# Optimization experiments

Hardware: AMD Instinct MI355X
Metric: run time of the kernel (lower is better)

## Reference

```python
import jax, jax.numpy as jnp
import numpy as np

B, T, C = 4, 2048, 2048
H, HKV, D = 16, 8, 128
SECTIONS = (24, 20, 20)  # sums to 64 = D/2 -> full-dim rotation branch
EPS = 1e-6


def setup_inputs() -> dict:
    key = jax.random.key(0)
    ks = jax.random.split(key, 8)
    x = jax.random.normal(ks[0], (B, T, C), dtype=jnp.float32)
    # realistic RoPE tables: [3, B, T, 64] (3 mRoPE axes: t/h/w)
    half = sum(SECTIONS)  # 64
    inv_freq = 1.0 / (10000.0 ** (jnp.arange(half, dtype=jnp.float32) / half))
    pos = jnp.arange(T, dtype=jnp.float32)
    freqs = pos[:, None] * inv_freq[None, :]                      # [T, 64]
    freqs3 = jnp.broadcast_to(freqs, (3, B, T, half))
    # small per-axis offsets so the three mRoPE axes differ
    axis_off = jnp.arange(3, dtype=jnp.float32)[:, None, None, None] * 0.5
    cos = jnp.cos(freqs3 + axis_off)
    sin = jnp.sin(freqs3 + axis_off)
    mask = jnp.ones((B, T), dtype=jnp.int32)
    s = 1.0 / np.sqrt(C)
    Wq = jax.random.normal(ks[1], (C, H * D), dtype=jnp.float32) * s
    Wk = jax.random.normal(ks[2], (C, HKV * D), dtype=jnp.float32) * s
    Wv = jax.random.normal(ks[3], (C, HKV * D), dtype=jnp.float32) * s
    Wo = jax.random.normal(ks[4], (H * D, C), dtype=jnp.float32) * (1.0 / np.sqrt(H * D))
    return dict(x=x, cos=cos, sin=sin, mask=mask,
                Wq=Wq, bq=jnp.zeros((H * D,), jnp.float32),
                Wk=Wk, bk=jnp.zeros((HKV * D,), jnp.float32),
                Wv=Wv, bv=jnp.zeros((HKV * D,), jnp.float32),
                gq=jnp.ones((D,), jnp.float32), gk=jnp.ones((D,), jnp.float32),
                Wo=Wo)


def _rms_norm(x, gamma, eps):
    var = jnp.mean(jnp.square(x.astype(jnp.float32)), axis=-1, keepdims=True)
    return (gamma * x * jax.lax.rsqrt(var + eps)).astype(x.dtype)


def _rotate_half(x):
    x1, x2 = jnp.split(x, 2, axis=-1)
    return jnp.concatenate((-x2, x1), axis=-1)


def _reorder(table):
    # interleave mRoPE sections: take section i from axis i, then duplicate
    chunks, off = [], 0
    for i, sec in enumerate(SECTIONS):
        chunks.append(table[i, ..., off:off + sec])
        off += sec
    r = jnp.concatenate(chunks, axis=-1)        # [B, T, 64]
    return jnp.concatenate([r, r], axis=-1)     # [B, T, 128]


def reference(x, cos, sin, mask, Wq, bq, Wk, bk, Wv, bv, gq, gk, Wo):
    b, t = x.shape[0], x.shape[1]
    q = (x @ Wq + bq).reshape(b, t, H, D)
    k = (x @ Wk + bk).reshape(b, t, HKV, D)
    v = (x @ Wv + bv).reshape(b, t, HKV, D)
    q = _rms_norm(q, gq, EPS)
    k = _rms_norm(k, gk, EPS)
    q = jnp.transpose(q, (0, 2, 1, 3))   # [B, H, T, D]
    k = jnp.transpose(k, (0, 2, 1, 3))   # [B, HKV, T, D]
    v = jnp.transpose(v, (0, 2, 1, 3))
    cos_e = _reorder(cos)[:, None].astype(q.dtype)  # [B, 1, T, D]
    sin_e = _reorder(sin)[:, None].astype(q.dtype)
    q = q * cos_e + _rotate_half(q) * sin_e
    k = k * cos_e + _rotate_half(k) * sin_e
    key_mask = mask.astype(jnp.float32)                         # [B, T]
    lengths = key_mask.sum(axis=-1).astype(jnp.int32)           # [B]
    k = k * key_mask[:, None, :, None].astype(k.dtype)
    v = v * key_mask[:, None, :, None].astype(v.dtype)
    history_mask = (jnp.arange(t)[None, :] < lengths[:, None]).astype(jnp.float32)
    repeats = H // HKV
    qg = q.reshape(b, HKV, repeats, t, D)
    scores = jnp.einsum('bhgqd,bhkd->bhgqk', qg.astype(jnp.float32),
                        k.astype(jnp.float32)) * D ** -0.5
    scores = scores.reshape(b, H, t, t)
    scores = scores + (1.0 - history_mask)[:, None, None, :] * -1e9
    causal = jnp.tril(jnp.ones((t, t), dtype=jnp.float32))
    scores = scores + (1.0 - causal)[None, None] * -1e9
    weights = jax.nn.softmax(scores, axis=-1)
    wg = weights.reshape(b, HKV, repeats, t, t)
    out = jnp.einsum('bhgqk,bhkd->bhgqd', wg, v.astype(jnp.float32))
    out = out.reshape(b, H, t, D).astype(x.dtype)
    out = jnp.transpose(out, (0, 2, 1, 3)).reshape(b, t, H * D)
    return out @ Wo
```

## Files before the change

### kernel.cpp

```cpp
#include <hip/hip_runtime.h>
#include <stdint.h>

#define B_    4
#define T_    2048
#define C_    2048
#define H_    16
#define HKV_  8
#define D_    128
#define HD_   2048
#define KVD_  1024
#define NQKV_ 4096
#define BT_   8192

typedef __bf16 bf16x8 __attribute__((ext_vector_type(8)));
typedef float  f32x4  __attribute__((ext_vector_type(4)));
typedef unsigned short u16;
typedef unsigned int   u32;

__device__ __forceinline__ u16 f2b(float f){
  union { float f; u32 u; } v; v.f = f;
  u32 r = v.u + 0x7FFFu + ((v.u >> 16) & 1u);
  return (u16)(r >> 16);
}
__device__ __forceinline__ float b2f(u16 h){
  union { u32 u; float f; } v; v.u = ((u32)h) << 16;
  return v.f;
}

#define GLOAD16(src, dst) __builtin_amdgcn_global_load_lds( \
    (const __attribute__((address_space(1))) u32*)(src), \
    (__attribute__((address_space(3))) u32*)(dst), 16, 0, 0)

#define MFMA16(a,b,c) __builtin_amdgcn_mfma_f32_16x16x32_bf16((a), (b), (c), 0, 0, 0)

__global__ __launch_bounds__(256) void k_convx(const float* __restrict__ x, u16* __restrict__ xb){
  size_t i = ((size_t)blockIdx.x * 256 + threadIdx.x) * 4;
  float4 v = *(const float4*)(x + i);
  u32 w0 = (u32)f2b(v.x) | ((u32)f2b(v.y) << 16);
  u32 w1 = (u32)f2b(v.z) | ((u32)f2b(v.w) << 16);
  uint2 pk; pk.x = w0; pk.y = w1;
  *(uint2*)(xb + i) = pk;
}

__global__ __launch_bounds__(256) void k_wtrans(const float* __restrict__ src, u16* __restrict__ dst,
                                                int K, int N){
  __shared__ __attribute__((aligned(16))) u16 tile[64][68];
  int n0 = blockIdx.x * 64, k0 = blockIdx.y * 64;
  int r = threadIdx.x >> 4, c4 = (threadIdx.x & 15) * 4;
  #pragma unroll
  for (int rr = 0; rr < 4; ++rr){
    int kl = r + rr * 16;
    float4 v = *(const float4*)(src + (size_t)(k0 + kl) * N + n0 + c4);
    tile[kl][c4+0] = f2b(v.x); tile[kl][c4+1] = f2b(v.y);
    tile[kl][c4+2] = f2b(v.z); tile[kl][c4+3] = f2b(v.w);
  }
  __syncthreads();
  #pragma unroll
  for (int rr = 0; rr < 4; ++rr){
    int nl = r + rr * 16;
    u32 w0 = (u32)tile[c4+0][nl] | ((u32)tile[c4+1][nl] << 16);
    u32 w1 = (u32)tile[c4+2][nl] | ((u32)tile[c4+3][nl] << 16);
    uint2 pk; pk.x = w0; pk.y = w1;
    *(uint2*)(dst + (size_t)(n0 + nl) * K + k0 + c4) = pk;
  }
}

__global__ void k_prep(const float* __restrict__ bq, const float* __restrict__ bk,
                       const float* __restrict__ bv, float* __restrict__ bias){
  int i = blockIdx.x * 256 + threadIdx.x;
  if (i < NQKV_)
    bias[i] = (i < HD_) ? bq[i] : (i < HD_ + KVD_ ? bk[i - HD_] : bv[i - HD_ - KVD_]);
}

__global__ void k_lens(const int* __restrict__ mask, int* __restrict__ lens){
  int b = blockIdx.x;
  int s = 0;
  for (int t = threadIdx.x; t < T_; t += 256) s += mask[b * T_ + t];
  #pragma unroll
  for (int d = 1; d < 64; d <<= 1) s += __shfl_xor(s, d);
  __shared__ int acc[4];
  if ((threadIdx.x & 63) == 0) acc[threadIdx.x >> 6] = s;
  __syncthreads();
  if (threadIdx.x == 0) lens[b] = acc[0] + acc[1] + acc[2] + acc[3];
}

template<bool OUTF32>
__global__ __launch_bounds__(256) void k_gemm(const u16* __restrict__ A, const u16* __restrict__ BT,
                                              const float* __restrict__ bias, void* __restrict__ Cout,
                                              int M, int N, int K, int nbx){
  __shared__ __attribute__((aligned(16))) u16 As[2][128 * 64];
  __shared__ __attribute__((aligned(16))) u16 Bs[2][128 * 64];
  int nwg = gridDim.x;
  int fid = blockIdx.x;
  int gs = (fid & 7) * (nwg >> 3) + (fid >> 3);
  int bx = gs % nbx, by = gs / nbx;
  int m0 = by * 128, n0 = bx * 128;
  int tid = threadIdx.x;
  int lane = tid & 63, w = tid >> 6;
  int wr = w >> 1, wc = w & 1;
  int g = lane >> 4, lo = lane & 15;
  int srow = lane >> 3;
  int sgr  = (lane & 7) ^ srow;
  int lsx  = (lo & 7) << 3;
  f32x4 acc[4][4] = {};

  auto STAGE = [&](int k0, int bufi){
    #pragma unroll
    for (int c = 0; c < 4; ++c){
      int ch = w * 4 + c;
      int row = ch * 8 + srow;
      GLOAD16(A + (size_t)(m0 + row) * K + k0 + sgr * 8, &As[bufi][ch * 512]);
    }
    #pragma unroll
    for (int c = 0; c < 4; ++c){
      int ch = w * 4 + c;
      int row = ch * 8 + srow;
      GLOAD16(BT + (size_t)(n0 + row) * K + k0 + sgr * 8, &Bs[bufi][ch * 512]);
    }
  };

  int nk = K >> 6;
  STAGE(0, 0);
  int cur = 0;
  for (int t = 0; t < nk; ++t){
    if (t + 1 < nk){
      STAGE((t + 1) * 64, cur ^ 1);
      asm volatile("s_waitcnt vmcnt(8)" ::: "memory");
    } else {
      asm volatile("s_waitcnt vmcnt(0)" ::: "memory");
    }
    __builtin_amdgcn_s_barrier();
    __builtin_amdgcn_sched_barrier(0);
    #pragma unroll
    for (int kk = 0; kk < 2; ++kk){
      bf16x8 af[4], bfv[4];
      #pragma unroll
      for (int i = 0; i < 4; ++i)
        af[i] = *(const bf16x8*)&As[cur][(wr*64 + i*16 + lo) * 64 + ((kk*32 + g*8) ^ lsx)];
      #pragma unroll
      for (int j = 0; j < 4; ++j)
        bfv[j] = *(const bf16x8*)&Bs[cur][(wc*64 + j*16 + lo) * 64 + ((kk*32 + g*8) ^ lsx)];
      __builtin_amdgcn_s_setprio(1);
      #pragma unroll
      for (int i = 0; i < 4; ++i)
        #pragma unroll
        for (int j = 0; j < 4; ++j)
          acc[i][j] = MFMA16(af[i], bfv[j], acc[i][j]);
      __builtin_amdgcn_s_setprio(0);
    }
    __builtin_amdgcn_s_barrier();
    cur ^= 1;
  }
  #pragma unroll
  for (int i = 0; i < 4; ++i){
    #pragma unroll
    for (int j = 0; j < 4; ++j){
      #pragma unroll
      for (int r = 0; r < 4; ++r){
        int row = m0 + wr*64 + i*16 + g*4 + r;
        int col = n0 + wc*64 + j*16 + lo;
        float v = acc[i][j][r] + (bias ? bias[col] : 0.0f);
        if (OUTF32) ((float*)Cout)[(size_t)row * N + col] = v;
        else        ((u16*)Cout)[(size_t)row * N + col] = f2b(v);
      }
    }
  }
}

__global__ __launch_bounds__(256) void k_rmsrope(const u16* __restrict__ qkv,
    const float* __restrict__ cosp, const float* __restrict__ sinp,
    const int* __restrict__ mask, const float* __restrict__ gq, const float* __restrict__ gk,
    u16* __restrict__ qrot, u16* __restrict__ krot){
  const float QS = 0.08838834764831845f * 1.4426950408889634f;
  int tok = blockIdx.x;
  int b = tok >> 11, t = tok & (T_ - 1);
  int lane = threadIdx.x & 63, w = threadIdx.x >> 6;
  int dl = (lane & 31) * 2;
  int a0 = dl < 24 ? 0 : (dl < 44 ? 1 : 2);
  int a1 = (dl + 1) < 24 ? 0 : ((dl + 1) < 44 ? 1 : 2);
  size_t cb = ((size_t)b * T_ + t) * 64;
  const size_t AX = (size_t)B_ * T_ * 64;
  float ce0 = cosp[(size_t)a0 * AX + cb + dl],     se0 = sinp[(size_t)a0 * AX + cb + dl];
  float ce1 = cosp[(size_t)a1 * AX + cb + dl + 1], se1 = sinp[(size_t)a1 * AX + cb + dl + 1];
  float sgn = (lane < 32) ? -1.f : 1.f;
  float mk = (float)mask[b * T_ + t];
  const u16* base = qkv + (size_t)tok * NQKV_;
  for (int head = w; head < H_ + HKV_; head += 4){
    bool isq = head < H_;
    int off = isq ? head * D_ : HD_ + (head - H_) * D_;
    u32 pr = *(const u32*)(base + off + lane * 2);
    float x0 = b2f((u16)(pr & 0xFFFF)), x1 = b2f((u16)(pr >> 16));
    float ss = x0*x0 + x1*x1;
    #pragma unroll
    for (int d = 1; d < 64; d <<= 1) ss += __shfl_xor(ss, d);
    float rinv = rsqrtf(ss * (1.0f / 128.0f) + 1e-6f);
    const float* gg = isq ? gq : gk;
    float2 gv = *(const float2*)(gg + lane * 2);
    float n0 = gv.x * x0 * rinv, n1 = gv.y * x1 * rinv;
    float p0 = __shfl_xor(n0, 32), p1 = __shfl_xor(n1, 32);
    float o0 = n0 * ce0 + sgn * p0 * se0;
    float o1 = n1 * ce1 + sgn * p1 * se1;
    u16* dst;
    if (isq){
      o0 *= QS; o1 *= QS;
      dst = qrot + ((size_t)(b * H_ + head) * T_ + t) * D_;
    } else {
      o0 *= mk; o1 *= mk;
      dst = krot + ((size_t)(b * HKV_ + (head - H_)) * T_ + t) * D_;
    }
    u32 ow = (u32)f2b(o0) | ((u32)f2b(o1) << 16);
    *(u32*)(dst + lane * 2) = ow;
  }
}

__global__ __launch_bounds__(256) void k_vtrans(const u16* __restrict__ qkv, const int* __restrict__ mask,
                                                u16* __restrict__ vt){
  int t0 = blockIdx.x * 64, d0 = blockIdx.y * 64;
  int bh = blockIdx.z;
  int b = bh >> 3, hk = bh & 7;
  __shared__ __attribute__((aligned(16))) u16 tile[64][68];
  int r = threadIdx.x >> 4, c4 = (threadIdx.x & 15) * 4;
  #pragma unroll
  for (int rr = 0; rr < 4; ++rr){
    int tl = r + rr * 16;
    int t = t0 + tl;
    u16 mz = (u16)(mask[b * T_ + t] ? 0xFFFFu : 0u);
    ushort4 v = *(const ushort4*)(qkv + (size_t)(b * T_ + t) * NQKV_ + HD_ + KVD_ + hk * D_ + d0 + c4);
    tile[tl][c4+0] = (u16)(v.x & mz); tile[tl][c4+1] = (u16)(v.y & mz);
    tile[tl][c4+2] = (u16)(v.z & mz); tile[tl][c4+3] = (u16)(v.w & mz);
  }
  __syncthreads();
  #pragma unroll
  for (int rr = 0; rr < 4; ++rr){
    int dn = r + rr * 16;
    u32 w0 = (u32)tile[c4+0][dn] | ((u32)tile[c4+1][dn] << 16);
    u32 w1 = (u32)tile[c4+2][dn] | ((u32)tile[c4+3][dn] << 16);
    uint2 pk; pk.x = w0; pk.y = w1;
    *(uint2*)(vt + ((size_t)bh * D_ + d0 + dn) * T_ + t0 + c4) = pk;
  }
}

__global__ __launch_bounds__(512) void k_attn(const u16* __restrict__ qrot, const u16* __restrict__ krot,
                                              const u16* __restrict__ vt, const int* __restrict__ lens,
                                              u16* __restrict__ ao){
  int fid = blockIdx.x;
  int gs = (fid & 7) * 128 + (fid >> 3);
  int qi = (gs & 15) ^ 15;
  int q0 = qi * 128;
  int h = (gs >> 4) & 15, b = gs >> 8;
  int hk = h >> 1;
  int tid = threadIdx.x;
  int lane = tid & 63, w = tid >> 6;
  int g = lane >> 4, lo = lane & 15;
  int len = lens[b];
  __shared__ __attribute__((aligned(16))) u16 Ks[2][64 * 128];
  __shared__ __attribute__((aligned(16))) u16 Vs[2][128 * 64];
  const u16* qbase = qrot + ((size_t)(b * H_ + h) * T_ + q0 + w * 16 + lo) * D_ + g * 8;
  bf16x8 qf[4];
  #pragma unroll
  for (int kk = 0; kk < 4; ++kk) qf[kk] = *(const bf16x8*)(qbase + kk * 32);
  float m_run = -1e30f, l_run = 0.f;
  f32x4 o[8] = {};
  int qrow = q0 + w * 16 + lo;
  const u16* kbase = krot + (size_t)(b * HKV_ + hk) * T_ * D_;
  const u16* vbase = vt   + (size_t)(b * HKV_ + hk) * D_ * T_;
  int wbase = tid & 448;
  int lsx = (lo & 7) << 3;
  int srcA = ((lane & 16) * 2 + lo) * 4;
  int srcB = srcA + 64;
  bool hiL = lane >= 32;

  auto STAGE = [&](int j0, int bufi){
    #pragma unroll
    for (int i = 0; i < 2; ++i){
      int gI = i * 512 + tid;
      int row = gI >> 4, grp = gI & 15;
      GLOAD16(kbase + (size_t)(j0 + row) * D_ + ((grp ^ (row & 7)) << 3),
              &Ks[bufi][(i * 512 + wbase) * 8]);
    }
    #pragma unroll
    for (int i = 0; i < 2; ++i){
      int gI = i * 512 + tid;
      int row = gI >> 3, grp = gI & 7;
      GLOAD16(vbase + (size_t)row * T_ + j0 + ((grp ^ (row & 7)) << 3),
              &Vs[bufi][(i * 512 + wbase) * 8]);
    }
  };

  STAGE(0, 0);
  int cur = 0;
  int jend = q0 + 64;
  for (int j0 = 0; j0 <= jend && j0 < len; j0 += 64){
    int jn = j0 + 64;
    bool hasnext = (jn <= jend && jn < len);
    if (hasnext){
      STAGE(jn, cur ^ 1);
      asm volatile("s_waitcnt vmcnt(4)" ::: "memory");
    } else {
      asm volatile("s_waitcnt vmcnt(0)" ::: "memory");
    }
    __builtin_amdgcn_s_barrier();
    __builtin_amdgcn_sched_barrier(0);
    bool wlive = (j0 <= q0 + w * 16 + 15);
    if (wlive){
      f32x4 st[4] = {};
      __builtin_amdgcn_s_setprio(1);
      #pragma unroll
      for (int kk = 0; kk < 4; ++kk){
        #pragma unroll
        for (int nf = 0; nf < 4; ++nf){
          bf16x8 kf = *(const bf16x8*)&Ks[cur][(nf * 16 + lo) * 128 + ((kk * 32 + g * 8) ^ lsx)];
          st[nf] = MFMA16(kf, qf[kk], st[nf]);
        }
      }
      __builtin_amdgcn_s_setprio(0);
      bool needmask = (j0 + 63 > q0 + w * 16) || (j0 + 64 > len);
      if (needmask){
        #pragma unroll
        for (int nf = 0; nf < 4; ++nf)
          #pragma unroll
          for (int r = 0; r < 4; ++r){
            int k = j0 + nf * 16 + g * 4 + r;
            if (k > qrow || k >= len) st[nf][r] = -1e30f;
          }
      }
      float mf[4];
      #pragma unroll
      for (int nf = 0; nf < 4; ++nf)
        mf[nf] = fmaxf(fmaxf(st[nf][0], st[nf][1]), fmaxf(st[nf][2], st[nf][3]));
      float mx = fmaxf(fmaxf(mf[0], mf[1]), fmaxf(mf[2], mf[3]));
      mx = fmaxf(mx, __shfl_xor(mx, 16));
      mx = fmaxf(mx, __shfl_xor(mx, 32));
      bool skip = __all(mx <= m_run + 8.0f);
      float mn = skip ? m_run : fmaxf(m_run, mx);
      float sf[4];
      #pragma unroll
      for (int nf = 0; nf < 4; ++nf){
        #pragma unroll
        for (int r = 0; r < 4; ++r){
          float e = exp2f(st[nf][r] - mn);
          st[nf][r] = e;
        }
        sf[nf] = (st[nf][0] + st[nf][1]) + (st[nf][2] + st[nf][3]);
      }
      float sum = (sf[0] + sf[1]) + (sf[2] + sf[3]);
      sum += __shfl_xor(sum, 16);
      sum += __shfl_xor(sum, 32);
      if (skip){
        l_run += sum;
      } else {
        float alpha = exp2f(m_run - mn);
        l_run = l_run * alpha + sum;
        m_run = mn;
        #pragma unroll
        for (int r = 0; r < 4; ++r){
          float ar = __shfl(alpha, (lane & 48) | ((g * 4 + r) & 15));
          #pragma unroll
          for (int df = 0; df < 8; ++df) o[df][r] *= ar;
        }
      }
      u32 pk[4][2];
      #pragma unroll
      for (int nf = 0; nf < 4; ++nf){
        union { u32 u; __bf16 hh[2]; } c0, c1;
        c0.hh[0] = (__bf16)st[nf][0]; c0.hh[1] = (__bf16)st[nf][1];
        c1.hh[0] = (__bf16)st[nf][2]; c1.hh[1] = (__bf16)st[nf][3];
        pk[nf][0] = c0.u; pk[nf][1] = c1.u;
      }
      #pragma unroll
      for (int kk2 = 0; kk2 < 2; ++kk2){
        u32 a0 = (u32)__builtin_amdgcn_ds_bpermute(srcA, (int)pk[2*kk2][0]);
        u32 b0 = (u32)__builtin_amdgcn_ds_bpermute(srcA, (int)pk[2*kk2+1][0]);
        u32 a1 = (u32)__builtin_amdgcn_ds_bpermute(srcA, (int)pk[2*kk2][1]);
        u32 b1 = (u32)__builtin_amdgcn_ds_bpermute(srcA, (int)pk[2*kk2+1][1]);
        u32 a2 = (u32)__builtin_amdgcn_ds_bpermute(srcB, (int)pk[2*kk2][0]);
        u32 b2 = (u32)__builtin_amdgcn_ds_bpermute(srcB, (int)pk[2*kk2+1][0]);
        u32 a3 = (u32)__builtin_amdgcn_ds_bpermute(srcB, (int)pk[2*kk2][1]);
        u32 b3 = (u32)__builtin_amdgcn_ds_bpermute(srcB, (int)pk[2*kk2+1][1]);
        union { u32 u[4]; bf16x8 v; } pf;
        pf.u[0] = hiL ? b0 : a0;
        pf.u[1] = hiL ? b1 : a1;
        pf.u[2] = hiL ? b2 : a2;
        pf.u[3] = hiL ? b3 : a3;
        __builtin_amdgcn_s_setprio(1);
        #pragma unroll
        for (int df = 0; df < 8; ++df){
          bf16x8 vf = *(const bf16x8*)&Vs[cur][(df * 16 + lo) * 64 + ((kk2 * 32 + g * 8) ^ lsx)];
          o[df] = MFMA16(pf.v, vf, o[df]);
        }
        __builtin_amdgcn_s_setprio(0);
      }
    }
    __builtin_amdgcn_s_barrier();
    cur ^= 1;
  }
  #pragma unroll
  for (int r = 0; r < 4; ++r){
    float lr = __shfl(l_run, (lane & 48) | ((g * 4 + r) & 15));
    float rl = 1.0f / lr;
    int row = q0 + w * 16 + g * 4 + r;
    #pragma unroll
    for (int df = 0; df < 8; ++df){
      float ov = o[df][r] * rl;
      ao[((size_t)(b * T_ + row)) * HD_ + h * D_ + df * 16 + lo] = f2b(ov);
    }
  }
}

extern "C" void kernel_launch(void* const* d_in, const int* in_sizes, int n_in,
                              void* d_out, int out_size, void* d_ws, size_t ws_size,
                              hipStream_t stream) {
  (void)in_sizes; (void)n_in; (void)out_size; (void)ws_size;
  const float* x    = (const float*)d_in[0];
  const float* cosp = (const float*)d_in[1];
  const float* sinp = (const float*)d_in[2];
  const int*   mask = (const int*)d_in[3];
  const float* Wq   = (const float*)d_in[4];
  const float* bq   = (const float*)d_in[5];
  const float* Wk   = (const float*)d_in[6];
  const float* bk   = (const float*)d_in[7];
  const float* Wv   = (const float*)d_in[8];
  const float* bv   = (const float*)d_in[9];
  const float* gq   = (const float*)d_in[10];
  const float* gk   = (const float*)d_in[11];
  const float* Wo   = (const float*)d_in[12];

  char* ws = (char*)d_ws;
  const size_t MB = 1024 * 1024;
  u16*   XB    = (u16*)(ws);
  u16*   WQKVT = (u16*)(ws + 32  * MB);
  u16*   WOT   = (u16*)(ws + 48  * MB);
  u16*   QKV   = (u16*)(ws + 56  * MB);
  u16*   QROT  = (u16*)(ws + 120 * MB);
  u16*   KROT  = (u16*)(ws + 152 * MB);
  u16*   VT    = (u16*)(ws + 168 * MB);
  u16*   AO    = (u16*)(ws + 184 * MB);
  float* BIAS  = (float*)(ws + 216 * MB);
  int*   LENS  = (int*)(ws + 216 * MB + 65536);

  k_convx<<<16384, 256, 0, stream>>>(x, XB);
  k_wtrans<<<dim3(32, 32), 256, 0, stream>>>(Wq, WQKVT, C_, HD_);
  k_wtrans<<<dim3(16, 32), 256, 0, stream>>>(Wk, WQKVT + (size_t)HD_ * C_, C_, KVD_);
  k_wtrans<<<dim3(16, 32), 256, 0, stream>>>(Wv, WQKVT + (size_t)(HD_ + KVD_) * C_, C_, KVD_);
  k_wtrans<<<dim3(32, 32), 256, 0, stream>>>(Wo, WOT, HD_, C_);
  k_prep<<<16, 256, 0, stream>>>(bq, bk, bv, BIAS);
  k_lens<<<4, 256, 0, stream>>>(mask, LENS);

  k_gemm<false><<<2048, 256, 0, stream>>>(XB, WQKVT, BIAS, QKV, BT_, NQKV_, C_, 32);
  k_rmsrope<<<BT_, 256, 0, stream>>>(QKV, cosp, sinp, mask, gq, gk, QROT, KROT);
  k_vtrans<<<dim3(T_ / 64, D_ / 64, B_ * HKV_), 256, 0, stream>>>(QKV, mask, VT);
  k_attn<<<1024, 512, 0, stream>>>(QROT, KROT, VT, LENS, AO);
  k_gemm<true><<<1024, 256, 0, stream>>>(AO, WOT, nullptr, d_out, BT_, C_, HD_, 16);
}
```

Measured before the change: 528.0 us.

## Enlarge GEMM tiles to 256x256 with 8 waves and phased prefetch

The bf16 GEMM kernel moves from 128x128 tiles with 4 waves to 256x256 tiles with 8 waves, each wave computing a 128x64 sub-tile. The next K-slice load is split into four quarter stages interleaved with the four MFMA phases, each phase separated by barriers. This aims to raise arithmetic intensity per LDS and global load and to overlap memory traffic with compute. In exchange it uses 128KB of LDS per block, more accumulator registers, extra barriers per iteration, and produces far fewer blocks (512 and 256), which could leave the 256 CUs poorly balanced.

```diff
diff --git a/kernel.cpp b/kernel.cpp
--- a/kernel.cpp
+++ b/kernel.cpp
@@ -85,81 +85,95 @@
 }
 
 template<bool OUTF32>
-__global__ __launch_bounds__(256) void k_gemm(const u16* __restrict__ A, const u16* __restrict__ BT,
-                                              const float* __restrict__ bias, void* __restrict__ Cout,
-                                              int M, int N, int K, int nbx){
-  __shared__ __attribute__((aligned(16))) u16 As[2][128 * 64];
-  __shared__ __attribute__((aligned(16))) u16 Bs[2][128 * 64];
+__global__ __launch_bounds__(512, 2) void k_gemm(const u16* __restrict__ A, const u16* __restrict__ BT,
+                                                 const float* __restrict__ bias, void* __restrict__ Cout,
+                                                 int M, int N, int K, int nbx){
+  __shared__ __attribute__((aligned(16))) u16 As[2][256 * 64];
+  __shared__ __attribute__((aligned(16))) u16 Bs[2][256 * 64];
   int nwg = gridDim.x;
   int fid = blockIdx.x;
   int gs = (fid & 7) * (nwg >> 3) + (fid >> 3);
   int bx = gs % nbx, by = gs / nbx;
-  int m0 = by * 128, n0 = bx * 128;
+  int m0 = by * 256, n0 = bx * 256;
   int tid = threadIdx.x;
   int lane = tid & 63, w = tid >> 6;
-  int wr = w >> 1, wc = w & 1;
+  int wm = w >> 2, wn = w & 3;
   int g = lane >> 4, lo = lane & 15;
-  int srow = lane >> 3;
-  int sgr  = (lane & 7) ^ srow;
-  int lsx  = (lo & 7) << 3;
-  f32x4 acc[4][4] = {};
-
-  auto STAGE = [&](int k0, int bufi){
-    #pragma unroll
-    for (int c = 0; c < 4; ++c){
-      int ch = w * 4 + c;
-      int row = ch * 8 + srow;
-      GLOAD16(A + (size_t)(m0 + row) * K + k0 + sgr * 8, &As[bufi][ch * 512]);
-    }
-    #pragma unroll
-    for (int c = 0; c < 4; ++c){
-      int ch = w * 4 + c;
-      int row = ch * 8 + srow;
-      GLOAD16(BT + (size_t)(n0 + row) * K + k0 + sgr * 8, &Bs[bufi][ch * 512]);
+  int lsx = (lo & 7) << 3;
+  int wgb = tid & 448;
+  f32x4 acc[8][4] = {};
+
+  auto STAGE_HALF = [&](const u16* __restrict__ src, int k0, u16* lds){
+    #pragma unroll
+    for (int i = 0; i < 2; ++i){
+      int gI = i * 512 + tid;
+      int row = gI >> 3, grp = gI & 7;
+      GLOAD16(src + (size_t)row * K + k0 + ((grp ^ (row & 7)) << 3),
+              &lds[(i * 512 + wgb) * 8]);
     }
   };
 
   int nk = K >> 6;
-  STAGE(0, 0);
-  int cur = 0;
+  STAGE_HALF(A  + (size_t)m0 * K,          0, &As[0][0]);
+  STAGE_HALF(A  + (size_t)(m0 + 128) * K,  0, &As[0][8192]);
+  STAGE_HALF(BT + (size_t)n0 * K,          0, &Bs[0][0]);
+  STAGE_HALF(BT + (size_t)(n0 + 128) * K,  0, &Bs[0][8192]);
+
   for (int t = 0; t < nk; ++t){
-    if (t + 1 < nk){
-      STAGE((t + 1) * 64, cur ^ 1);
-      asm volatile("s_waitcnt vmcnt(8)" ::: "memory");
-    } else {
-      asm volatile("s_waitcnt vmcnt(0)" ::: "memory");
-    }
-    __builtin_amdgcn_s_barrier();
-    __builtin_amdgcn_sched_barrier(0);
-    #pragma unroll
-    for (int kk = 0; kk < 2; ++kk){
-      bf16x8 af[4], bfv[4];
-      #pragma unroll
-      for (int i = 0; i < 4; ++i)
-        af[i] = *(const bf16x8*)&As[cur][(wr*64 + i*16 + lo) * 64 + ((kk*32 + g*8) ^ lsx)];
-      #pragma unroll
-      for (int j = 0; j < 4; ++j)
-        bfv[j] = *(const bf16x8*)&Bs[cur][(wc*64 + j*16 + lo) * 64 + ((kk*32 + g*8) ^ lsx)];
+    int cur = t & 1, nxt = cur ^ 1;
+    bool pf = (t + 1 < nk);
+    int kn = (t + 1) * 64;
+    bf16x8 bfr[4][2];
+    #pragma unroll
+    for (int p = 0; p < 4; ++p){
+      if (p == 0){
+        if (pf){
+          STAGE_HALF(A + (size_t)m0 * K, kn, &As[nxt][0]);
+          asm volatile("s_waitcnt vmcnt(2)" ::: "memory");
+        } else {
+          asm volatile("s_waitcnt vmcnt(0)" ::: "memory");
+        }
+        __builtin_amdgcn_s_barrier();
+        #pragma unroll
+        for (int nr = 0; nr < 4; ++nr){
+          bfr[nr][0] = *(const bf16x8*)&Bs[cur][(wn*64 + nr*16 + lo) * 64 + ((0*32 + g*8) ^ lsx)];
+          bfr[nr][1] = *(const bf16x8*)&Bs[cur][(wn*64 + nr*16 + lo) * 64 + ((1*32 + g*8) ^ lsx)];
+        }
+      } else {
+        if (pf){
+          if (p == 1) STAGE_HALF(A  + (size_t)(m0 + 128) * K, kn, &As[nxt][8192]);
+          if (p == 2) STAGE_HALF(BT + (size_t)n0 * K,         kn, &Bs[nxt][0]);
+          if (p == 3) STAGE_HALF(BT + (size_t)(n0 + 128) * K, kn, &Bs[nxt][8192]);
+        }
+        __builtin_amdgcn_s_barrier();
+      }
+      int r0 = 2 * p, r1 = 2 * p + 1;
+      bf16x8 a00 = *(const bf16x8*)&As[cur][(wm*128 + r0*16 + lo) * 64 + ((0*32 + g*8) ^ lsx)];
+      bf16x8 a01 = *(const bf16x8*)&As[cur][(wm*128 + r0*16 + lo) * 64 + ((1*32 + g*8) ^ lsx)];
+      bf16x8 a10 = *(const bf16x8*)&As[cur][(wm*128 + r1*16 + lo) * 64 + ((0*32 + g*8) ^ lsx)];
+      bf16x8 a11 = *(const bf16x8*)&As[cur][(wm*128 + r1*16 + lo) * 64 + ((1*32 + g*8) ^ lsx)];
+      __builtin_amdgcn_sched_barrier(0);
       __builtin_amdgcn_s_setprio(1);
       #pragma unroll
-      for (int i = 0; i < 4; ++i)
-        #pragma unroll
-        for (int j = 0; j < 4; ++j)
-          acc[i][j] = MFMA16(af[i], bfv[j], acc[i][j]);
+      for (int nr = 0; nr < 4; ++nr){
+        acc[r0][nr] = MFMA16(a00, bfr[nr][0], acc[r0][nr]);
+        acc[r0][nr] = MFMA16(a01, bfr[nr][1], acc[r0][nr]);
+        acc[r1][nr] = MFMA16(a10, bfr[nr][0], acc[r1][nr]);
+        acc[r1][nr] = MFMA16(a11, bfr[nr][1], acc[r1][nr]);
+      }
       __builtin_amdgcn_s_setprio(0);
-    }
-    __builtin_amdgcn_s_barrier();
-    cur ^= 1;
-  }
-  #pragma unroll
-  for (int i = 0; i < 4; ++i){
-    #pragma unroll
-    for (int j = 0; j < 4; ++j){
+      __builtin_amdgcn_s_barrier();
+    }
+  }
+  #pragma unroll
+  for (int mr = 0; mr < 8; ++mr){
+    #pragma unroll
+    for (int nr = 0; nr < 4; ++nr){
       #pragma unroll
       for (int r = 0; r < 4; ++r){
-        int row = m0 + wr*64 + i*16 + g*4 + r;
-        int col = n0 + wc*64 + j*16 + lo;
-        float v = acc[i][j][r] + (bias ? bias[col] : 0.0f);
+        int row = m0 + wm*128 + mr*16 + g*4 + r;
+        int col = n0 + wn*64 + nr*16 + lo;
+        float v = acc[mr][nr][r] + (bias ? bias[col] : 0.0f);
         if (OUTF32) ((float*)Cout)[(size_t)row * N + col] = v;
         else        ((u16*)Cout)[(size_t)row * N + col] = f2b(v);
       }
@@ -446,9 +460,9 @@
   k_prep<<<16, 256, 0, stream>>>(bq, bk, bv, BIAS);
   k_lens<<<4, 256, 0, stream>>>(mask, LENS);
 
-  k_gemm<false><<<2048, 256, 0, stream>>>(XB, WQKVT, BIAS, QKV, BT_, NQKV_, C_, 32);
+  k_gemm<false><<<512, 512, 0, stream>>>(XB, WQKVT, BIAS, QKV, BT_, NQKV_, C_, 16);
   k_rmsrope<<<BT_, 256, 0, stream>>>(QKV, cosp, sinp, mask, gq, gk, QROT, KROT);
   k_vtrans<<<dim3(T_ / 64, D_ / 64, B_ * HKV_), 256, 0, stream>>>(QKV, mask, VT);
   k_attn<<<1024, 512, 0, stream>>>(QROT, KROT, VT, LENS, AO);
-  k_gemm<true><<<1024, 256, 0, stream>>>(AO, WOT, nullptr, d_out, BT_, C_, HD_, 16);
-}
+  k_gemm<true><<<256, 512, 0, stream>>>(AO, WOT, nullptr, d_out, BT_, C_, HD_, 8);
+}
```

Result: no change. 524.5 us (-0.7%).
